# Kernel optimization log

Hardware: AMD Instinct MI355X
Metric: run time of the kernel (lower is better)

## Reference

```python
import jax, jax.numpy as jnp
import numpy as np

BATCH = 2048
DIM = 1024       # discrete_dim
EMBED = 512
HID = 2 * EMBED  # MLP hidden width per source: [embed_dim*2, embed_dim*2, discrete_dim]
NUM_STEPS = 32


def setup_inputs() -> dict:
    key = jax.random.key(0)
    ks = jax.random.split(key, 8)
    s = 0.02  # init scale for weights
    init_samples = jax.random.randint(ks[0], (BATCH, DIM), 0, 2).astype(jnp.float32)
    target_pos = jax.random.randint(ks[1], (NUM_STEPS, BATCH), 0, DIM, dtype=jnp.int32)
    W1 = jax.random.normal(ks[2], (DIM, HID), jnp.float32) * s
    b1 = jnp.zeros((HID,), jnp.float32)
    W2 = jax.random.normal(ks[3], (HID, HID), jnp.float32) * s
    b2 = jnp.zeros((HID,), jnp.float32)
    W3 = jax.random.normal(ks[4], (HID, DIM), jnp.float32) * s
    b3 = jnp.zeros((DIM,), jnp.float32)
    return {
        "init_samples": init_samples, "target_pos": target_pos,
        "W1": W1, "b1": b1, "W2": W2, "b2": b2, "W3": W3, "b3": b3,
        "num_steps": NUM_STEPS,
    }


def _mlp(x, W1, b1, W2, b2, W3, b3):
    h = jax.nn.relu(x @ W1 + b1)
    h = jax.nn.relu(h @ W2 + b2)
    return h @ W3 + b3  # pos logits, [B, DIM]


def reference(init_samples, target_pos, W1, b1, W2, b2, W3, b3, num_steps):
    B = init_samples.shape[0]
    rows = jnp.arange(B)
    very_init_samples = init_samples
    total_log0 = jnp.zeros((B, 1), init_samples.dtype)  # mode != 'forward': total_log = 0.0

    def step(carry, tpos):
        samples, total_log = carry
        log_pos_prob = jax.nn.log_softmax(_mlp(samples, W1, b1, W2, b2, W3, b3), axis=-1)
        log_target = jnp.take_along_axis(log_pos_prob, tpos[:, None], axis=1)  # [B,1]
        total_log = total_log + log_target
        orig_bit = samples[rows, tpos]                       # gather, [B]
        samples = samples.at[rows, tpos].set(1.0 - orig_bit)  # scatter bit flip
        return (samples, total_log), tpos

    (final_samples, total_log), delta = jax.lax.scan(
        step, (init_samples, total_log0), target_pos[:num_steps])
    return final_samples, delta, total_log, very_init_samples
```

## Files before the change

kernel.cpp:

```cpp
#include <hip/hip_runtime.h>
#include <stdint.h>

#define BATCH 2048
#define NDIM  1024
#define HID   1024
#define TSTEPS 32

#define OUT_FINAL 0
#define OUT_DELTA 2097152
#define OUT_TOTAL 2162688
#define OUT_VINIT 2164736

#define SC_ROWSUM 0
#define SC_TGT    8192
#define SC_TOTAL  16384
#define SC_BIAS   24576
#define SC_FLAG   36864

#define WF_WT1    0u
#define WF_WT2    2097152u
#define WF_WT3    4194304u
#define WF_A1     6291456u
#define WF_BIAS   14680064u
#define WF_SIGNS  14692352u
#define WF_ROWSUM 14757888u
#define WF_TGT    15020032u
#define WF_FLAG   15282176u
#define WF_H1     15286272u

__device__ __forceinline__ float bf2f(ushort u) {
  union { uint32_t u; float f; } v; v.u = ((uint32_t)u) << 16; return v.f;
}
__device__ __forceinline__ ushort f2bf(float f) {
  union { float f; uint32_t u; } v; v.f = f;
  uint32_t u = v.u;
  u += 0x7fffu + ((u >> 16) & 1u);
  return (ushort)(u >> 16);
}

typedef __attribute__((ext_vector_type(8))) short bf16x8;
typedef __attribute__((ext_vector_type(8))) unsigned short u16x8;
typedef __attribute__((ext_vector_type(4))) float f32x4;

__device__ __forceinline__ void gload_lds16(const void* g, void* l) {
  __builtin_amdgcn_global_load_lds((const __attribute__((address_space(1))) void*)g,
                                   (__attribute__((address_space(3))) void*)l, 16, 0, 0);
}

__global__ __launch_bounds__(256) void flag_k(const void* __restrict__ init,
                                              uint32_t* __restrict__ flag) {
  const ushort* p = (const ushort*)init;
  __shared__ uint32_t acc[256];
  uint32_t a = 0;
  for (int i = threadIdx.x; i < 32768; i += 256) a |= p[2 * i];
  acc[threadIdx.x] = a;
  __syncthreads();
  for (int s = 128; s > 0; s >>= 1) {
    if (threadIdx.x < s) acc[threadIdx.x] |= acc[threadIdx.x + s];
    __syncthreads();
  }
  if (threadIdx.x == 0) *flag = (acc[0] != 0) ? 1u : 0u;
}

__global__ __launch_bounds__(256) void zero_k(float* __restrict__ p) {
  p[blockIdx.x * 256 + threadIdx.x] = 0.f;
}

__global__ __launch_bounds__(256) void canon_b_k(const void* b1, const void* b2,
                                                 const void* b3,
                                                 float* __restrict__ dst,
                                                 const uint32_t* __restrict__ flag) {
  const void* src = (blockIdx.x == 0) ? b1 : (blockIdx.x == 1) ? b2 : b3;
  float* d = dst + blockIdx.x * 1024;
  const bool isbf = (*flag != 0);
  for (int i = threadIdx.x; i < 1024; i += 256)
    d[i] = isbf ? bf2f(((const ushort*)src)[i]) : ((const float*)src)[i];
}

__global__ __launch_bounds__(256) void canon_w_k(const void* __restrict__ S,
                                                 ushort* __restrict__ D,
                                                 const uint32_t* __restrict__ flag) {
  __shared__ ushort tile[32][33];
  const int bx = blockIdx.x * 32, by = blockIdx.y * 32;
  const int tx = threadIdx.x, ty = threadIdx.y;
  const bool isbf = (*flag != 0);
  #pragma unroll
  for (int i = 0; i < 32; i += 8) {
    const size_t idx = (size_t)(by + ty + i) * 1024 + bx + tx;
    tile[ty + i][tx] = isbf ? ((const ushort*)S)[idx] : f2bf(((const float*)S)[idx]);
  }
  __syncthreads();
  #pragma unroll
  for (int i = 0; i < 32; i += 8)
    D[(size_t)(bx + ty + i) * 1024 + by + tx] = tile[tx][ty + i];
}

__global__ __launch_bounds__(256) void sign_k(const void* __restrict__ init,
                                              const int* __restrict__ tpos,
                                              uint8_t* __restrict__ signs,
                                              const uint32_t* __restrict__ flag) {
  const int m = blockIdx.x, tid = threadIdx.x;
  const bool isbf = (*flag != 0);
  __shared__ float bits[NDIM];
  #pragma unroll
  for (int i = 0; i < 4; ++i) {
    const int k = tid + i * 256;
    bits[k] = isbf ? bf2f(((const ushort*)init)[(size_t)m * NDIM + k])
                   : ((const float*)init)[(size_t)m * NDIM + k];
  }
  __syncthreads();
  if (tid == 0) {
    for (int t = 0; t < TSTEPS; ++t) {
      const int tp = tpos[t * BATCH + m];
      const float b = bits[tp];
      signs[t * BATCH + m] = (uint8_t)(b != 0.f);
      bits[tp] = 1.f - b;
    }
  }
}

template <int ASTAGE, int EPI>
__global__ __launch_bounds__(256) void gemm_bt(const void* __restrict__ A,
                                               const ushort* __restrict__ Bt,
                                               const float* __restrict__ bias,
                                               void* __restrict__ Cout,
                                               const int* __restrict__ tpos,
                                               float* __restrict__ rowsum,
                                               float* __restrict__ tgt,
                                               const uint32_t* __restrict__ flag,
                                               int rowbase) {
  constexpr int BM = 128, BN = 128, BK = 32, K = 1024;
  __shared__ ushort Asm[BM * BK];
  __shared__ ushort Bsm[BN * BK];
  const int tid = threadIdx.x;
  const int wave = tid >> 6, lane = tid & 63;
  const int q = lane >> 4, r = lane & 15;

  const int lid = blockIdx.y * gridDim.x + blockIdx.x;
  const int xcd = lid & 7;
  const int s   = lid >> 3;
  const int mb  = xcd + 8 * (s >> 3);
  const int nb  = s & 7;
  const int n0 = nb * BN;
  const int m0 = mb * BM;
  const int wm = (wave & 1) * 64, wn = (wave >> 1) * 64;

  f32x4 acc[4][4];
  #pragma unroll
  for (int i = 0; i < 4; ++i)
    #pragma unroll
    for (int j = 0; j < 4; ++j)
      #pragma unroll
      for (int e = 0; e < 4; ++e) acc[i][j][e] = 0.f;

  const int f0 = tid * 16, f1 = f0 + 4096;
  const int row0 = f0 >> 6, kb0 = f0 & 63;
  const int row1 = f1 >> 6, kb1 = f1 & 63;
  const bool isbf = (ASTAGE == 1) ? (*flag != 0) : true;

  for (int k0 = 0; k0 < K; k0 += BK) {
    if constexpr (ASTAGE == 0) {
      gload_lds16((const char*)A + ((size_t)(m0 + row0) * K + k0) * 2 + kb0, (char*)Asm + f0);
      gload_lds16((const char*)A + ((size_t)(m0 + row1) * K + k0) * 2 + kb1, (char*)Asm + f1);
    } else {
      u16x8 a0, a1v;
      const int e0 = kb0 >> 1, e1 = kb1 >> 1;
      if (isbf) {
        a0  = *(const u16x8*)((const ushort*)A + (size_t)(m0 + row0) * K + k0 + e0);
        a1v = *(const u16x8*)((const ushort*)A + (size_t)(m0 + row1) * K + k0 + e1);
      } else {
        const float* p0 = (const float*)A + (size_t)(m0 + row0) * K + k0 + e0;
        const float* p1 = (const float*)A + (size_t)(m0 + row1) * K + k0 + e1;
        const float4 fa = *(const float4*)p0, fb = *(const float4*)(p0 + 4);
        const float4 fc = *(const float4*)p1, fd = *(const float4*)(p1 + 4);
        a0[0] = f2bf(fa.x); a0[1] = f2bf(fa.y); a0[2] = f2bf(fa.z); a0[3] = f2bf(fa.w);
        a0[4] = f2bf(fb.x); a0[5] = f2bf(fb.y); a0[6] = f2bf(fb.z); a0[7] = f2bf(fb.w);
        a1v[0] = f2bf(fc.x); a1v[1] = f2bf(fc.y); a1v[2] = f2bf(fc.z); a1v[3] = f2bf(fc.w);
        a1v[4] = f2bf(fd.x); a1v[5] = f2bf(fd.y); a1v[6] = f2bf(fd.z); a1v[7] = f2bf(fd.w);
      }
      *(u16x8*)((char*)Asm + f0) = a0;
      *(u16x8*)((char*)Asm + f1) = a1v;
    }
    gload_lds16((const char*)Bt + ((size_t)(n0 + row0) * K + k0) * 2 + kb0, (char*)Bsm + f0);
    gload_lds16((const char*)Bt + ((size_t)(n0 + row1) * K + k0) * 2 + kb1, (char*)Bsm + f1);
    __syncthreads();
    bf16x8 af[4], bfr[4];
    #pragma unroll
    for (int t = 0; t < 4; ++t) {
      af[t]  = *(const bf16x8*)(Asm + (wm + t * 16 + r) * BK + q * 8);
      bfr[t] = *(const bf16x8*)(Bsm + (wn + t * 16 + r) * BK + q * 8);
    }
    #pragma unroll
    for (int mt = 0; mt < 4; ++mt)
      #pragma unroll
      for (int nt = 0; nt < 4; ++nt)
        acc[mt][nt] = __builtin_amdgcn_mfma_f32_16x16x32_bf16(af[mt], bfr[nt], acc[mt][nt], 0, 0, 0);
    __syncthreads();
  }

  #pragma unroll
  for (int mt = 0; mt < 4; ++mt) {
    #pragma unroll
    for (int reg = 0; reg < 4; ++reg) {
      const int grow = m0 + wm + mt * 16 + q * 4 + reg;
      if constexpr (EPI == 2) {
        const int growg = rowbase + grow;
        const int tp = tpos[growg];
        float s2 = 0.f;
        #pragma unroll
        for (int nt = 0; nt < 4; ++nt) {
          const int gcol = n0 + wn + nt * 16 + r;
          const float v = acc[mt][nt][reg] + bias[gcol];
          if (gcol == tp) tgt[growg] = v;
          s2 += __expf(v);
        }
        s2 += __shfl_xor(s2, 1);
        s2 += __shfl_xor(s2, 2);
        s2 += __shfl_xor(s2, 4);
        s2 += __shfl_xor(s2, 8);
        if (r == 0) atomicAdd(&rowsum[growg], s2);
      } else {
        #pragma unroll
        for (int nt = 0; nt < 4; ++nt) {
          const int gcol = n0 + wn + nt * 16 + r;
          const float v = acc[mt][nt][reg] + bias[gcol];
          if constexpr (EPI == 0) {
            ((float*)Cout)[(size_t)grow * NDIM + gcol] = v;
          } else {
            ((ushort*)Cout)[(size_t)grow * NDIM + gcol] = f2bf(v > 0.f ? v : 0.f);
          }
        }
      }
    }
  }
}

__global__ __launch_bounds__(256) void build_h1(float* __restrict__ a1,
                                                const void* __restrict__ W1,
                                                const uint8_t* __restrict__ signs,
                                                const int* __restrict__ tpos,
                                                ushort* __restrict__ h1,
                                                const uint32_t* __restrict__ flag,
                                                int t0, int nsteps) {
  const int m = blockIdx.x;
  const int k = threadIdx.x * 4;
  const bool isbf = (*flag != 0);
  float4 a = *(const float4*)(a1 + (size_t)m * HID + k);
  for (int t = 0; t < nsteps; ++t) {
    ushort4 h;
    h.x = f2bf(a.x > 0.f ? a.x : 0.f);
    h.y = f2bf(a.y > 0.f ? a.y : 0.f);
    h.z = f2bf(a.z > 0.f ? a.z : 0.f);
    h.w = f2bf(a.w > 0.f ? a.w : 0.f);
    *(ushort4*)(h1 + ((size_t)(t * BATCH + m)) * HID + k) = h;
    const int tg = t0 + t;
    const int tp = tpos[tg * BATCH + m];
    const float s = 1.f - 2.f * (float)signs[tg * BATCH + m];
    float wx, wy, wz, ww;
    if (isbf) {
      const ushort4 wv = *(const ushort4*)((const ushort*)W1 + (size_t)tp * HID + k);
      wx = bf2f(wv.x); wy = bf2f(wv.y); wz = bf2f(wv.z); ww = bf2f(wv.w);
    } else {
      const float4 wv = *(const float4*)((const float*)W1 + (size_t)tp * HID + k);
      wx = wv.x; wy = wv.y; wz = wv.z; ww = wv.w;
    }
    a.x += s * wx; a.y += s * wy; a.z += s * wz; a.w += s * ww;
  }
  *(float4*)(a1 + (size_t)m * HID + k) = a;
}

__global__ __launch_bounds__(256) void fin_total_k(const float* __restrict__ tgt,
                                                   const float* __restrict__ rowsum,
                                                   float* __restrict__ out_total) {
  const int m = blockIdx.x * 256 + threadIdx.x;
  float acc = 0.f;
  for (int t = 0; t < TSTEPS; ++t) {
    const int rr = t * BATCH + m;
    acc += tgt[rr] - logf(rowsum[rr]);
  }
  out_total[m] = acc;
}

template <int ASRC, int EPI>
__global__ __launch_bounds__(256) void gemm_t(const void* __restrict__ A,
                                              const void* __restrict__ W,
                                              const float* __restrict__ bias,
                                              ushort* __restrict__ Cout,
                                              const int* __restrict__ tpos,
                                              float* __restrict__ rowsum,
                                              float* __restrict__ tgt,
                                              const uint32_t* __restrict__ flag,
                                              int tstep) {
  constexpr int BM = 64, BN = 64, BK = 32, BKP = 40, K = 1024;
  __shared__ ushort Asm[BM * BKP];
  __shared__ ushort Bsm[BN * BKP];
  const int tid = threadIdx.x;
  const int w = tid >> 6, lane = tid & 63;
  const int q = lane >> 4, r = lane & 15;
  const int n0 = blockIdx.x * BN;
  const int m0 = blockIdx.y * BM;
  const bool isbf = (*flag != 0);
  const int srow = tid >> 2, scol = (tid & 3) * 8;
  const int kk = tid >> 3, ng = (tid & 7) * 8;

  f32x4 acc[4];
  #pragma unroll
  for (int nt = 0; nt < 4; ++nt)
    #pragma unroll
    for (int e = 0; e < 4; ++e) acc[nt][e] = 0.f;

  for (int k0 = 0; k0 < K; k0 += BK) {
    u16x8 av;
    if constexpr (ASRC == 0) {
      if (isbf) {
        av = *(const u16x8*)((const ushort*)A + (size_t)(m0 + srow) * K + k0 + scol);
      } else {
        const float* fp = (const float*)A + (size_t)(m0 + srow) * K + k0 + scol;
        const float4 fa = *(const float4*)fp, fb = *(const float4*)(fp + 4);
        av[0] = f2bf(fa.x); av[1] = f2bf(fa.y); av[2] = f2bf(fa.z); av[3] = f2bf(fa.w);
        av[4] = f2bf(fb.x); av[5] = f2bf(fb.y); av[6] = f2bf(fb.z); av[7] = f2bf(fb.w);
      }
    } else {
      av = *(const u16x8*)((const ushort*)A + (size_t)(m0 + srow) * K + k0 + scol);
      if constexpr (ASRC == 1) {
        #pragma unroll
        for (int e = 0; e < 8; ++e) av[e] = (av[e] & 0x8000u) ? (unsigned short)0 : av[e];
      }
    }
    ushort bw[8];
    if (isbf) {
      const u16x8 wv = *(const u16x8*)((const ushort*)W + (size_t)(k0 + kk) * NDIM + n0 + ng);
      #pragma unroll
      for (int j = 0; j < 8; ++j) bw[j] = wv[j];
    } else {
      const float* fp = (const float*)W + (size_t)(k0 + kk) * NDIM + n0 + ng;
      const float4 fa = *(const float4*)fp, fb = *(const float4*)(fp + 4);
      bw[0] = f2bf(fa.x); bw[1] = f2bf(fa.y); bw[2] = f2bf(fa.z); bw[3] = f2bf(fa.w);
      bw[4] = f2bf(fb.x); bw[5] = f2bf(fb.y); bw[6] = f2bf(fb.z); bw[7] = f2bf(fb.w);
    }
    __syncthreads();
    *(u16x8*)(Asm + srow * BKP + scol) = av;
    #pragma unroll
    for (int j = 0; j < 8; ++j) Bsm[(ng + j) * BKP + kk] = bw[j];
    __syncthreads();
    const bf16x8 af = *(const bf16x8*)(Asm + (w * 16 + r) * BKP + q * 8);
    #pragma unroll
    for (int nt = 0; nt < 4; ++nt) {
      const bf16x8 bfr = *(const bf16x8*)(Bsm + (nt * 16 + r) * BKP + q * 8);
      acc[nt] = __builtin_amdgcn_mfma_f32_16x16x32_bf16(af, bfr, acc[nt], 0, 0, 0);
    }
  }

  if constexpr (EPI == 2) {
    #pragma unroll
    for (int reg = 0; reg < 4; ++reg) {
      const int grow = m0 + w * 16 + q * 4 + reg;
      const int tp = tpos[tstep * BATCH + grow];
      float s = 0.f;
      #pragma unroll
      for (int nt = 0; nt < 4; ++nt) {
        const int gcol = n0 + nt * 16 + r;
        const float v = acc[nt][reg] + bias[gcol];
        if (gcol == tp) tgt[grow] = v;
        s += __expf(v);
      }
      s += __shfl_xor(s, 1);
      s += __shfl_xor(s, 2);
      s += __shfl_xor(s, 4);
      s += __shfl_xor(s, 8);
      if (r == 0) atomicAdd(&rowsum[grow], s);
    }
  } else {
    #pragma unroll
    for (int nt = 0; nt < 4; ++nt) {
      #pragma unroll
      for (int reg = 0; reg < 4; ++reg) {
        const int grow = m0 + w * 16 + q * 4 + reg;
        const int gcol = n0 + nt * 16 + r;
        float v = acc[nt][reg] + bias[gcol];
        if constexpr (EPI == 1) v = (v > 0.f) ? v : 0.f;
        Cout[(size_t)grow * NDIM + gcol] = f2bf(v);
      }
    }
  }
}

__global__ __launch_bounds__(256) void step_k(ushort* __restrict__ a1,
                                              const void* __restrict__ init,
                                              const void* __restrict__ W1,
                                              const int* __restrict__ tpos,
                                              float* __restrict__ rowsum,
                                              const float* __restrict__ tgt,
                                              float* __restrict__ total,
                                              const uint32_t* __restrict__ flag,
                                              int t) {
  const int m = blockIdx.x;
  const int k = threadIdx.x * 4;
  const bool isbf = (*flag != 0);
  const int tp = tpos[t * BATCH + m];
  const float b0 = isbf ? bf2f(((const ushort*)init)[(size_t)m * NDIM + tp])
                        : ((const float*)init)[(size_t)m * NDIM + tp];
  int cnt = 0;
  for (int u = 0; u < t; ++u) cnt += (tpos[u * BATCH + m] == tp) ? 1 : 0;
  const float bit = (cnt & 1) ? (1.f - b0) : b0;
  const float s = 1.f - 2.f * bit;
  float wx, wy, wz, ww;
  if (isbf) {
    const ushort4 wv = *(const ushort4*)((const ushort*)W1 + (size_t)tp * HID + k);
    wx = bf2f(wv.x); wy = bf2f(wv.y); wz = bf2f(wv.z); ww = bf2f(wv.w);
  } else {
    const float4 wv = *(const float4*)((const float*)W1 + (size_t)tp * HID + k);
    wx = wv.x; wy = wv.y; wz = wv.z; ww = wv.w;
  }
  ushort4 a = *(const ushort4*)(a1 + (size_t)m * HID + k);
  a.x = f2bf(bf2f(a.x) + s * wx);
  a.y = f2bf(bf2f(a.y) + s * wy);
  a.z = f2bf(bf2f(a.z) + s * wz);
  a.w = f2bf(bf2f(a.w) + s * ww);
  *(ushort4*)(a1 + (size_t)m * HID + k) = a;
  if (threadIdx.x == 0) {
    total[m] += tgt[m] - logf(rowsum[m]);
    rowsum[m] = 0.f;
  }
}

__global__ __launch_bounds__(256) void finalize_k(const float* __restrict__ total,
                                                  float* __restrict__ out_total) {
  const int m = blockIdx.x * 256 + threadIdx.x;
  out_total[m] = total[m];
}

__global__ __launch_bounds__(256) void out_final_k(const void* __restrict__ init,
                                                   const int* __restrict__ tpos,
                                                   float* __restrict__ out,
                                                   const uint32_t* __restrict__ flag) {
  const int m = blockIdx.x;
  const int k = threadIdx.x * 4;
  const bool isbf = (*flag != 0);
  float v[4];
  if (isbf) {
    const ushort4 iv = *(const ushort4*)((const ushort*)init + (size_t)m * NDIM + k);
    v[0] = bf2f(iv.x); v[1] = bf2f(iv.y); v[2] = bf2f(iv.z); v[3] = bf2f(iv.w);
  } else {
    const float4 iv = *(const float4*)((const float*)init + (size_t)m * NDIM + k);
    v[0] = iv.x; v[1] = iv.y; v[2] = iv.z; v[3] = iv.w;
  }
  for (int t = 0; t < TSTEPS; ++t) {
    const int tp = tpos[t * BATCH + m];
    if ((tp >> 2) == (int)threadIdx.x) v[tp & 3] = 1.f - v[tp & 3];
  }
  float4 o; o.x = v[0]; o.y = v[1]; o.z = v[2]; o.w = v[3];
  *(float4*)(out + OUT_FINAL + (size_t)m * NDIM + k) = o;
}

__global__ __launch_bounds__(256) void out_vinit_k(const void* __restrict__ init,
                                                   float* __restrict__ out,
                                                   const uint32_t* __restrict__ flag) {
  const int i = (blockIdx.x * 256 + threadIdx.x) * 4;
  float4 o;
  if (*flag) {
    const ushort4 iv = *(const ushort4*)((const ushort*)init + i);
    o.x = bf2f(iv.x); o.y = bf2f(iv.y); o.z = bf2f(iv.z); o.w = bf2f(iv.w);
  } else {
    o = *(const float4*)((const float*)init + i);
  }
  *(float4*)(out + OUT_VINIT + i) = o;
}

__global__ __launch_bounds__(256) void out_delta_k(const int* __restrict__ tpos,
                                                   float* __restrict__ out) {
  const int i = blockIdx.x * 256 + threadIdx.x;
  out[OUT_DELTA + i] = (float)tpos[i];
}

extern "C" void kernel_launch(void* const* d_in, const int* in_sizes, int n_in,
                              void* d_out, int out_size, void* d_ws, size_t ws_size,
                              hipStream_t stream) {
  const void* init = d_in[0];
  const int* tpos  = (const int*)d_in[1];
  const void* W1 = d_in[2];
  const void* b1 = d_in[3];
  const void* W2 = d_in[4];
  const void* b2 = d_in[5];
  const void* W3 = d_in[6];
  const void* b3 = d_in[7];
  float* out = (float*)d_out;
  char* ws = (char*)d_ws;

  const size_t MB = 1024ull * 1024ull;
  int CH = TSTEPS;
  while (CH > 1 && (size_t)WF_H1 + (size_t)CH * 8 * MB > ws_size) CH >>= 1;
  const bool fast = (ws_size >= (size_t)WF_H1 + 8 * MB);

  if (fast) {
    ushort*   WT1    = (ushort*)(ws + WF_WT1);
    ushort*   WT2    = (ushort*)(ws + WF_WT2);
    ushort*   WT3    = (ushort*)(ws + WF_WT3);
    float*    a1f    = (float*)(ws + WF_A1);
    float*    biases = (float*)(ws + WF_BIAS);
    uint8_t*  signs  = (uint8_t*)(ws + WF_SIGNS);
    float*    rowsum = (float*)(ws + WF_ROWSUM);
    float*    tgt    = (float*)(ws + WF_TGT);
    uint32_t* flag   = (uint32_t*)(ws + WF_FLAG);
    ushort*   h1     = (ushort*)(ws + WF_H1);
    ushort*   h2     = (ushort*)(ws + WF_H1 + (size_t)CH * 4 * MB);

    flag_k<<<1, 256, 0, stream>>>(init, flag);
    canon_b_k<<<3, 256, 0, stream>>>(b1, b2, b3, biases, flag);
    canon_w_k<<<dim3(32, 32), dim3(32, 8), 0, stream>>>(W1, WT1, flag);
    canon_w_k<<<dim3(32, 32), dim3(32, 8), 0, stream>>>(W2, WT2, flag);
    canon_w_k<<<dim3(32, 32), dim3(32, 8), 0, stream>>>(W3, WT3, flag);
    sign_k<<<BATCH, 256, 0, stream>>>(init, tpos, signs, flag);
    zero_k<<<512, 256, 0, stream>>>(rowsum);

    gemm_bt<1, 0><<<dim3(8, 16), 256, 0, stream>>>(init, WT1, biases + 0, a1f,
                                                   nullptr, nullptr, nullptr, flag, 0);

    for (int t0 = 0; t0 < TSTEPS; t0 += CH) {
      build_h1<<<BATCH, 256, 0, stream>>>(a1f, W1, signs, tpos, h1, flag, t0, CH);
      gemm_bt<0, 1><<<dim3(8, CH * 16), 256, 0, stream>>>(h1, WT2, biases + 1024, h2,
                                                          nullptr, nullptr, nullptr, flag, 0);
      gemm_bt<0, 2><<<dim3(8, CH * 16), 256, 0, stream>>>(h2, WT3, biases + 2048, nullptr,
                                                          tpos, rowsum, tgt, flag, t0 * BATCH);
    }
    fin_total_k<<<8, 256, 0, stream>>>(tgt, rowsum, out + OUT_TOTAL);
    out_final_k<<<BATCH, 256, 0, stream>>>(init, tpos, out, flag);
    out_vinit_k<<<2048, 256, 0, stream>>>(init, out, flag);
    out_delta_k<<<256, 256, 0, stream>>>(tpos, out);
  } else {
    ushort*   a1     = (ushort*)(out + OUT_FINAL);
    ushort*   h2     = (ushort*)(out + OUT_VINIT);
    char*     sc     = (char*)(out + OUT_DELTA);
    float*    rowsum = (float*)(sc + SC_ROWSUM);
    float*    tgt    = (float*)(sc + SC_TGT);
    float*    total  = (float*)(sc + SC_TOTAL);
    float*    biases = (float*)(sc + SC_BIAS);
    uint32_t* flag   = (uint32_t*)(sc + SC_FLAG);

    flag_k<<<1, 256, 0, stream>>>(init, flag);
    zero_k<<<24, 256, 0, stream>>>(rowsum);
    canon_b_k<<<3, 256, 0, stream>>>(b1, b2, b3, biases, flag);
    gemm_t<0, 0><<<dim3(16, 32), 256, 0, stream>>>(init, W1, biases + 0, a1,
                                                   nullptr, nullptr, nullptr, flag, 0);
    for (int t = 0; t < TSTEPS; ++t) {
      gemm_t<1, 1><<<dim3(16, 32), 256, 0, stream>>>(a1, W2, biases + 1024, h2,
                                                     nullptr, nullptr, nullptr, flag, 0);
      gemm_t<2, 2><<<dim3(16, 32), 256, 0, stream>>>(h2, W3, biases + 2048, nullptr,
                                                     tpos, rowsum, tgt, flag, t);
      step_k<<<BATCH, 256, 0, stream>>>(a1, init, W1, tpos, rowsum, tgt, total, flag, t);
    }
    finalize_k<<<8, 256, 0, stream>>>(total, out + OUT_TOTAL);
    out_final_k<<<BATCH, 256, 0, stream>>>(init, tpos, out, flag);
    out_vinit_k<<<2048, 256, 0, stream>>>(init, out, flag);
    out_delta_k<<<256, 256, 0, stream>>>(tpos, out);
  }
}
```

Measured before the change: 606.2 us.

## Double GEMM K-tile to 64 with XOR-swizzled LDS layout, merge weight transposes

Raises the GEMM K-tile from 32 to 64, so each block does half as many barrier-separated load/compute iterations and runs two MFMA sub-steps per tile. Adds an XOR swizzle of the 16-byte chunks in the LDS A/B tiles to avoid bank conflicts on the fragment reads. Also merges the three weight transpose/convert launches into one 3D-grid launch, which relies on WT1..WT3 being contiguous 1M-element regions. LDS use doubles to 32 KB per block, which may reduce occupancy.

```diff
diff --git a/kernel.cpp b/kernel.cpp
--- a/kernel.cpp
+++ b/kernel.cpp
@@ -77,10 +77,14 @@
     d[i] = isbf ? bf2f(((const ushort*)src)[i]) : ((const float*)src)[i];
 }
 
-__global__ __launch_bounds__(256) void canon_w_k(const void* __restrict__ S,
-                                                 ushort* __restrict__ D,
-                                                 const uint32_t* __restrict__ flag) {
+__global__ __launch_bounds__(256) void canon_w3_k(const void* __restrict__ S1,
+                                                  const void* __restrict__ S2,
+                                                  const void* __restrict__ S3,
+                                                  ushort* __restrict__ D,
+                                                  const uint32_t* __restrict__ flag) {
   __shared__ ushort tile[32][33];
+  const void* S = (blockIdx.z == 0) ? S1 : (blockIdx.z == 1) ? S2 : S3;
+  ushort* Dz = D + (size_t)blockIdx.z * 1024 * 1024;
   const int bx = blockIdx.x * 32, by = blockIdx.y * 32;
   const int tx = threadIdx.x, ty = threadIdx.y;
   const bool isbf = (*flag != 0);
@@ -92,7 +96,7 @@
   __syncthreads();
   #pragma unroll
   for (int i = 0; i < 32; i += 8)
-    D[(size_t)(bx + ty + i) * 1024 + by + tx] = tile[tx][ty + i];
+    Dz[(size_t)(bx + ty + i) * 1024 + by + tx] = tile[tx][ty + i];
 }
 
 __global__ __launch_bounds__(256) void sign_k(const void* __restrict__ init,
@@ -129,7 +133,7 @@
                                                float* __restrict__ tgt,
                                                const uint32_t* __restrict__ flag,
                                                int rowbase) {
-  constexpr int BM = 128, BN = 128, BK = 32, K = 1024;
+  constexpr int BM = 128, BN = 128, BK = 64, K = 1024;
   __shared__ ushort Asm[BM * BK];
   __shared__ ushort Bsm[BN * BK];
   const int tid = threadIdx.x;
@@ -138,9 +142,9 @@
 
   const int lid = blockIdx.y * gridDim.x + blockIdx.x;
   const int xcd = lid & 7;
-  const int s   = lid >> 3;
-  const int mb  = xcd + 8 * (s >> 3);
-  const int nb  = s & 7;
+  const int sl  = lid >> 3;
+  const int mb  = xcd + 8 * (sl >> 3);
+  const int nb  = sl & 7;
   const int n0 = nb * BN;
   const int m0 = mb * BM;
   const int wm = (wave & 1) * 64, wn = (wave >> 1) * 64;
@@ -153,48 +157,61 @@
       #pragma unroll
       for (int e = 0; e < 4; ++e) acc[i][j][e] = 0.f;
 
-  const int f0 = tid * 16, f1 = f0 + 4096;
-  const int row0 = f0 >> 6, kb0 = f0 & 63;
-  const int row1 = f1 >> 6, kb1 = f1 & 63;
+  int srow[4], ssrc[4], sdst[4];
+  #pragma unroll
+  for (int j = 0; j < 4; ++j) {
+    const int f = j * 4096 + tid * 16;
+    const int rw = f >> 7;
+    const int c  = (f & 127) >> 4;
+    srow[j] = rw;
+    ssrc[j] = (c ^ (rw & 7)) * 8;
+    sdst[j] = f;
+  }
   const bool isbf = (ASTAGE == 1) ? (*flag != 0) : true;
 
   for (int k0 = 0; k0 < K; k0 += BK) {
     if constexpr (ASTAGE == 0) {
-      gload_lds16((const char*)A + ((size_t)(m0 + row0) * K + k0) * 2 + kb0, (char*)Asm + f0);
-      gload_lds16((const char*)A + ((size_t)(m0 + row1) * K + k0) * 2 + kb1, (char*)Asm + f1);
+      #pragma unroll
+      for (int j = 0; j < 4; ++j)
+        gload_lds16((const char*)A + ((size_t)(m0 + srow[j]) * K + k0 + ssrc[j]) * 2,
+                    (char*)Asm + sdst[j]);
     } else {
-      u16x8 a0, a1v;
-      const int e0 = kb0 >> 1, e1 = kb1 >> 1;
-      if (isbf) {
-        a0  = *(const u16x8*)((const ushort*)A + (size_t)(m0 + row0) * K + k0 + e0);
-        a1v = *(const u16x8*)((const ushort*)A + (size_t)(m0 + row1) * K + k0 + e1);
-      } else {
-        const float* p0 = (const float*)A + (size_t)(m0 + row0) * K + k0 + e0;
-        const float* p1 = (const float*)A + (size_t)(m0 + row1) * K + k0 + e1;
-        const float4 fa = *(const float4*)p0, fb = *(const float4*)(p0 + 4);
-        const float4 fc = *(const float4*)p1, fd = *(const float4*)(p1 + 4);
-        a0[0] = f2bf(fa.x); a0[1] = f2bf(fa.y); a0[2] = f2bf(fa.z); a0[3] = f2bf(fa.w);
-        a0[4] = f2bf(fb.x); a0[5] = f2bf(fb.y); a0[6] = f2bf(fb.z); a0[7] = f2bf(fb.w);
-        a1v[0] = f2bf(fc.x); a1v[1] = f2bf(fc.y); a1v[2] = f2bf(fc.z); a1v[3] = f2bf(fc.w);
-        a1v[4] = f2bf(fd.x); a1v[5] = f2bf(fd.y); a1v[6] = f2bf(fd.z); a1v[7] = f2bf(fd.w);
-      }
-      *(u16x8*)((char*)Asm + f0) = a0;
-      *(u16x8*)((char*)Asm + f1) = a1v;
-    }
-    gload_lds16((const char*)Bt + ((size_t)(n0 + row0) * K + k0) * 2 + kb0, (char*)Bsm + f0);
-    gload_lds16((const char*)Bt + ((size_t)(n0 + row1) * K + k0) * 2 + kb1, (char*)Bsm + f1);
+      u16x8 avv[4];
+      #pragma unroll
+      for (int j = 0; j < 4; ++j) {
+        if (isbf) {
+          avv[j] = *(const u16x8*)((const ushort*)A + (size_t)(m0 + srow[j]) * K + k0 + ssrc[j]);
+        } else {
+          const float* fp = (const float*)A + (size_t)(m0 + srow[j]) * K + k0 + ssrc[j];
+          const float4 fa = *(const float4*)fp, fb = *(const float4*)(fp + 4);
+          avv[j][0] = f2bf(fa.x); avv[j][1] = f2bf(fa.y); avv[j][2] = f2bf(fa.z); avv[j][3] = f2bf(fa.w);
+          avv[j][4] = f2bf(fb.x); avv[j][5] = f2bf(fb.y); avv[j][6] = f2bf(fb.z); avv[j][7] = f2bf(fb.w);
+        }
+      }
+      #pragma unroll
+      for (int j = 0; j < 4; ++j) *(u16x8*)((char*)Asm + sdst[j]) = avv[j];
+    }
+    #pragma unroll
+    for (int j = 0; j < 4; ++j)
+      gload_lds16((const char*)Bt + ((size_t)(n0 + srow[j]) * K + k0 + ssrc[j]) * 2,
+                  (char*)Bsm + sdst[j]);
     __syncthreads();
-    bf16x8 af[4], bfr[4];
-    #pragma unroll
-    for (int t = 0; t < 4; ++t) {
-      af[t]  = *(const bf16x8*)(Asm + (wm + t * 16 + r) * BK + q * 8);
-      bfr[t] = *(const bf16x8*)(Bsm + (wn + t * 16 + r) * BK + q * 8);
-    }
-    #pragma unroll
-    for (int mt = 0; mt < 4; ++mt)
-      #pragma unroll
-      for (int nt = 0; nt < 4; ++nt)
-        acc[mt][nt] = __builtin_amdgcn_mfma_f32_16x16x32_bf16(af[mt], bfr[nt], acc[mt][nt], 0, 0, 0);
+    #pragma unroll
+    for (int s = 0; s < 2; ++s) {
+      bf16x8 af[4], bfr[4];
+      #pragma unroll
+      for (int t = 0; t < 4; ++t) {
+        const int ra = wm + t * 16 + r;
+        af[t]  = *(const bf16x8*)(Asm + ra * BK + (((s * 4 + q) ^ (ra & 7)) * 8));
+        const int rb = wn + t * 16 + r;
+        bfr[t] = *(const bf16x8*)(Bsm + rb * BK + (((s * 4 + q) ^ (rb & 7)) * 8));
+      }
+      #pragma unroll
+      for (int mt = 0; mt < 4; ++mt)
+        #pragma unroll
+        for (int nt = 0; nt < 4; ++nt)
+          acc[mt][nt] = __builtin_amdgcn_mfma_f32_16x16x32_bf16(af[mt], bfr[nt], acc[mt][nt], 0, 0, 0);
+    }
     __syncthreads();
   }
 
@@ -507,9 +524,7 @@
 
     flag_k<<<1, 256, 0, stream>>>(init, flag);
     canon_b_k<<<3, 256, 0, stream>>>(b1, b2, b3, biases, flag);
-    canon_w_k<<<dim3(32, 32), dim3(32, 8), 0, stream>>>(W1, WT1, flag);
-    canon_w_k<<<dim3(32, 32), dim3(32, 8), 0, stream>>>(W2, WT2, flag);
-    canon_w_k<<<dim3(32, 32), dim3(32, 8), 0, stream>>>(W3, WT3, flag);
+    canon_w3_k<<<dim3(32, 32, 3), dim3(32, 8), 0, stream>>>(W1, W2, W3, WT1, flag);
     sign_k<<<BATCH, 256, 0, stream>>>(init, tpos, signs, flag);
     zero_k<<<512, 256, 0, stream>>>(rowsum);
 
```

New measurement: 592.7 us. -2.2%, faster.
